# Kernel optimization log

Measured on AMD Instinct MI355X. Metric: run time of the kernel, lower is better.

## Reference

```python
import jax, jax.numpy as jnp
import numpy as np

BATCH, SEQ, D_IN, D_OUT, PALETTE = 4, 2048, 4096, 4096, 256


def setup_inputs() -> dict:
    key = jax.random.key(0)
    k_in, k_w, k_lut, k_b = jax.random.split(key, 4)
    inp = jax.random.normal(k_in, (BATCH, SEQ, D_IN), dtype=jnp.float32)
    # palette indices playing the role of the stored uint8 weight tensor
    weight = jax.random.randint(k_w, (D_OUT, D_IN), 0, PALETTE, dtype=jnp.int32)
    # fp8-derived palette values (simulated as small fp32 centroids)
    lookup_table = jax.random.normal(k_lut, (PALETTE,), dtype=jnp.float32) * 0.02
    bias = jax.random.normal(k_b, (D_OUT,), dtype=jnp.float32) * 0.01
    return {"input": inp, "lookup_table": lookup_table, "weight": weight, "bias": bias}


def reference(input, lookup_table, weight, bias):
    # Dequantize palette indices -> full weight matrix [D_OUT, D_IN]
    full_weights = lookup_table[weight]
    # F.linear: input @ W^T + bias
    out = jnp.einsum("bsd,od->bso", input, full_weights)
    return out + bias
```

## Files before the change

kernel.cpp:

```cpp
#include <hip/hip_runtime.h>
#include <cstdint>


static constexpr int Md = 8192;
static constexpr int Nd = 4096;
static constexpr int Kd = 4096;

typedef _Float16 half8 __attribute__((ext_vector_type(8)));
typedef float f32x4 __attribute__((ext_vector_type(4)));

__device__ __forceinline__ void async_copy16(const _Float16* g, _Float16* l) {
  __builtin_amdgcn_global_load_lds((const __attribute__((address_space(1))) void*)g,
                                   (__attribute__((address_space(3))) void*)l, 16, 0, 0);
}

__global__ __launch_bounds__(256) void cvt_a(const float* __restrict__ in,
                                             _Float16* __restrict__ out) {
  const size_t i = (size_t)blockIdx.x * 256 + threadIdx.x;
  const float4 x = ((const float4*)in)[2 * i];
  const float4 y = ((const float4*)in)[2 * i + 1];
  half8 h;
  h[0] = (_Float16)x.x; h[1] = (_Float16)x.y; h[2] = (_Float16)x.z; h[3] = (_Float16)x.w;
  h[4] = (_Float16)y.x; h[5] = (_Float16)y.y; h[6] = (_Float16)y.z; h[7] = (_Float16)y.w;
  *(half8*)(out + 8 * i) = h;
}

__global__ __launch_bounds__(256) void dequant_b(const int* __restrict__ w,
                                                 const float* __restrict__ lut,
                                                 _Float16* __restrict__ out) {
  __shared__ float slut[256];
  slut[threadIdx.x] = lut[threadIdx.x];
  __syncthreads();
  const size_t i = (size_t)blockIdx.x * 256 + threadIdx.x;
  const int4 a = ((const int4*)w)[2 * i];
  const int4 b = ((const int4*)w)[2 * i + 1];
  half8 h;
  h[0] = (_Float16)slut[a.x]; h[1] = (_Float16)slut[a.y];
  h[2] = (_Float16)slut[a.z]; h[3] = (_Float16)slut[a.w];
  h[4] = (_Float16)slut[b.x]; h[5] = (_Float16)slut[b.y];
  h[6] = (_Float16)slut[b.z]; h[7] = (_Float16)slut[b.w];
  *(half8*)(out + 8 * i) = h;
}

__global__ __launch_bounds__(256) void gemm_f16(const _Float16* __restrict__ A,
                                                const _Float16* __restrict__ Bt,
                                                const float* __restrict__ bias,
                                                float* __restrict__ C) {
  __shared__ __align__(16) _Float16 As[128 * 64];
  __shared__ __align__(16) _Float16 Bs[128 * 64];

  const int tid = threadIdx.x;
  const int lane = tid & 63;
  const int wave = tid >> 6;
  const int wm = wave >> 1;
  const int wn = wave & 1;
  const int bm = blockIdx.x, bn = blockIdx.y;

  const int sr = wave * 8 + (lane >> 3);
  const int gc = ((lane & 7) ^ (sr & 7)) * 8;
  const _Float16* ag = A  + (size_t)(bm * 128 + sr) * Kd + gc;
  const _Float16* bg = Bt + (size_t)(bn * 128 + sr) * Kd + gc;
  _Float16* al = As + sr * 64 + (lane & 7) * 8;
  _Float16* bl = Bs + sr * 64 + (lane & 7) * 8;

  const int fr = lane & 15;
  const int fq = lane >> 4;
  const int e = fr & 7;
  const int slot0 = (fq ^ e) * 8;
  const int slot1 = ((4 | fq) ^ e) * 8;
  const _Float16* afp = As + (wm * 64 + fr) * 64;
  const _Float16* bfp = Bs + (wn * 64 + fr) * 64;

  f32x4 acc[4][4] = {};

  for (int kt = 0; kt < Kd / 64; ++kt) {
#pragma unroll
    for (int r = 0; r < 4; ++r) {
      async_copy16(ag + (size_t)r * 32 * Kd, al + r * 2048);
      async_copy16(bg + (size_t)r * 32 * Kd, bl + r * 2048);
    }
    ag += 64;
    bg += 64;
    __syncthreads();
#pragma unroll
    for (int ks = 0; ks < 2; ++ks) {
      const int slot = ks ? slot1 : slot0;
      half8 a[4], b[4];
#pragma unroll
      for (int i = 0; i < 4; ++i) a[i] = *(const half8*)(afp + i * 16 * 64 + slot);
#pragma unroll
      for (int j = 0; j < 4; ++j) b[j] = *(const half8*)(bfp + j * 16 * 64 + slot);
#pragma unroll
      for (int i = 0; i < 4; ++i)
#pragma unroll
        for (int j = 0; j < 4; ++j)
          acc[i][j] = __builtin_amdgcn_mfma_f32_16x16x32_f16(a[i], b[j], acc[i][j], 0, 0, 0);
    }
    __syncthreads();
  }

  const int ccol0 = bn * 128 + wn * 64 + fr;
  const int crow0 = bm * 128 + wm * 64 + fq * 4;
  float bv[4];
#pragma unroll
  for (int j = 0; j < 4; ++j) bv[j] = bias[ccol0 + j * 16];
#pragma unroll
  for (int i = 0; i < 4; ++i) {
#pragma unroll
    for (int r = 0; r < 4; ++r) {
      float* cp = C + (size_t)(crow0 + i * 16 + r) * Nd + ccol0;
#pragma unroll
      for (int j = 0; j < 4; ++j) cp[j * 16] = acc[i][j][r] + bv[j];
    }
  }
}

extern "C" void kernel_launch(void* const* d_in, const int* in_sizes, int n_in,
                              void* d_out, int out_size, void* d_ws, size_t ws_size,
                              hipStream_t stream) {
  const float* inp  = (const float*)d_in[0];
  const float* lut  = (const float*)d_in[1];
  const int*   wgt  = (const int*)d_in[2];
  const float* bias = (const float*)d_in[3];
  float* out = (float*)d_out;

  _Float16* Ah = (_Float16*)d_ws;
  _Float16* Bh = (_Float16*)d_ws + (size_t)Md * Kd;

  cvt_a<<<(Md * (size_t)Kd) / (8 * 256), 256, 0, stream>>>(inp, Ah);
  dequant_b<<<((size_t)Nd * Kd) / (8 * 256), 256, 0, stream>>>(wgt, lut, Bh);

  dim3 grid(Md / 128, Nd / 128);
  gemm_f16<<<grid, 256, 0, stream>>>(Ah, Bh, bias, out);
}
```

Before: 547.5 us.

## Use 256x256 tiles with double-buffered LDS and ping-pong MFMA scheduling

Replaces the 128x128 single-buffered GEMM with a 256x256 block tile of 512 threads. The LDS is double-buffered, so the next K-tile's async global-to-LDS copy is issued before the current tile is computed, with explicit waitcnt and barriers. The MFMA work is split into four quadrant phases with setprio so loads and matrix ops from the two resident blocks interleave, and a block-index remap groups blocks for L2 locality. The larger tile increases data reuse per loaded byte, at the cost of 128 KB of LDS per block, more accumulator registers, and many extra barriers.

```diff
diff --git a/kernel.cpp b/kernel.cpp
--- a/kernel.cpp
+++ b/kernel.cpp
@@ -5,6 +5,7 @@
 static constexpr int Md = 8192;
 static constexpr int Nd = 4096;
 static constexpr int Kd = 4096;
+static constexpr int NKT = Kd / 64;
 
 typedef _Float16 half8 __attribute__((ext_vector_type(8)));
 typedef float f32x4 __attribute__((ext_vector_type(4)));
@@ -42,70 +43,147 @@
   *(half8*)(out + 8 * i) = h;
 }
 
-__global__ __launch_bounds__(256) void gemm_f16(const _Float16* __restrict__ A,
-                                                const _Float16* __restrict__ Bt,
-                                                const float* __restrict__ bias,
-                                                float* __restrict__ C) {
-  __shared__ __align__(16) _Float16 As[128 * 64];
-  __shared__ __align__(16) _Float16 Bs[128 * 64];
+__global__ __launch_bounds__(512, 2) void gemm_f16(const _Float16* __restrict__ A,
+                                                   const _Float16* __restrict__ Bt,
+                                                   const float* __restrict__ bias,
+                                                   float* __restrict__ C) {
+  __shared__ __align__(16) _Float16 As[2][256 * 64];
+  __shared__ __align__(16) _Float16 Bs[2][256 * 64];
 
   const int tid = threadIdx.x;
   const int lane = tid & 63;
   const int wave = tid >> 6;
-  const int wm = wave >> 1;
-  const int wn = wave & 1;
-  const int bm = blockIdx.x, bn = blockIdx.y;
-
-  const int sr = wave * 8 + (lane >> 3);
-  const int gc = ((lane & 7) ^ (sr & 7)) * 8;
-  const _Float16* ag = A  + (size_t)(bm * 128 + sr) * Kd + gc;
-  const _Float16* bg = Bt + (size_t)(bn * 128 + sr) * Kd + gc;
-  _Float16* al = As + sr * 64 + (lane & 7) * 8;
-  _Float16* bl = Bs + sr * 64 + (lane & 7) * 8;
+  const int wm = wave >> 2;
+  const int wn = wave & 3;
+
+  const int bid0 = blockIdx.x + blockIdx.y * gridDim.x;
+  const int bid = (bid0 & 7) * 64 + (bid0 >> 3);
+  const int bm = bid & 31;
+  const int bn = bid >> 5;
+
+  const int trow = tid >> 3;
+  const int tcol = tid & 7;
+  const int gch = tcol ^ (trow & 7);
+  const _Float16* ag = A + (size_t)(bm * 256 + trow) * Kd + gch * 8;
+  const _Float16* bg = Bt + (size_t)(bn * 256 + trow) * Kd + gch * 8;
+  const int lds_off = trow * 64 + tcol * 8;
+
+  auto stage = [&](int buf, int kt) {
+#pragma unroll
+    for (int ht = 0; ht < 4; ++ht) {
+      async_copy16(ag + (size_t)kt * 64 + (size_t)ht * (64 * Kd),
+                   &As[buf][lds_off + ht * 4096]);
+      async_copy16(bg + (size_t)kt * 64 + (size_t)ht * (64 * Kd),
+                   &Bs[buf][lds_off + ht * 4096]);
+    }
+  };
 
   const int fr = lane & 15;
   const int fq = lane >> 4;
   const int e = fr & 7;
-  const int slot0 = (fq ^ e) * 8;
-  const int slot1 = ((4 | fq) ^ e) * 8;
-  const _Float16* afp = As + (wm * 64 + fr) * 64;
-  const _Float16* bfp = Bs + (wn * 64 + fr) * 64;
-
-  f32x4 acc[4][4] = {};
-
-  for (int kt = 0; kt < Kd / 64; ++kt) {
-#pragma unroll
-    for (int r = 0; r < 4; ++r) {
-      async_copy16(ag + (size_t)r * 32 * Kd, al + r * 2048);
-      async_copy16(bg + (size_t)r * 32 * Kd, bl + r * 2048);
-    }
-    ag += 64;
-    bg += 64;
-    __syncthreads();
-#pragma unroll
-    for (int ks = 0; ks < 2; ++ks) {
-      const int slot = ks ? slot1 : slot0;
-      half8 a[4], b[4];
-#pragma unroll
-      for (int i = 0; i < 4; ++i) a[i] = *(const half8*)(afp + i * 16 * 64 + slot);
-#pragma unroll
-      for (int j = 0; j < 4; ++j) b[j] = *(const half8*)(bfp + j * 16 * 64 + slot);
-#pragma unroll
-      for (int i = 0; i < 4; ++i)
-#pragma unroll
-        for (int j = 0; j < 4; ++j)
-          acc[i][j] = __builtin_amdgcn_mfma_f32_16x16x32_f16(a[i], b[j], acc[i][j], 0, 0, 0);
-    }
-    __syncthreads();
+  const int s0 = (fq ^ e) * 8;
+  const int s1 = ((4 | fq) ^ e) * 8;
+
+  f32x4 acc[8][4] = {};
+
+  stage(0, 0);
+
+  for (int kt = 0; kt < NKT; ++kt) {
+    const int cur = kt & 1;
+    if (kt + 1 < NKT) {
+      stage(cur ^ 1, kt + 1);
+      asm volatile("s_waitcnt vmcnt(8)" ::: "memory");
+    } else {
+      asm volatile("s_waitcnt vmcnt(0)" ::: "memory");
+    }
+    __builtin_amdgcn_s_barrier();
+
+    const _Float16* as = &As[cur][(wm * 128 + fr) * 64];
+    const _Float16* bs = &Bs[cur][(wn * 64 + fr) * 64];
+
+    half8 a[4][2], b0[2][2], b1[2][2];
+
+#pragma unroll
+    for (int i = 0; i < 4; ++i) {
+      a[i][0] = *(const half8*)(as + i * 16 * 64 + s0);
+      a[i][1] = *(const half8*)(as + i * 16 * 64 + s1);
+    }
+#pragma unroll
+    for (int j = 0; j < 2; ++j) {
+      b0[j][0] = *(const half8*)(bs + j * 16 * 64 + s0);
+      b0[j][1] = *(const half8*)(bs + j * 16 * 64 + s1);
+    }
+    __builtin_amdgcn_s_barrier();
+    asm volatile("s_waitcnt lgkmcnt(0)" ::: "memory");
+    __builtin_amdgcn_sched_barrier(0);
+    __builtin_amdgcn_s_setprio(1);
+#pragma unroll
+    for (int i = 0; i < 4; ++i)
+#pragma unroll
+      for (int j = 0; j < 2; ++j) {
+        acc[i][j] = __builtin_amdgcn_mfma_f32_16x16x32_f16(a[i][0], b0[j][0], acc[i][j], 0, 0, 0);
+        acc[i][j] = __builtin_amdgcn_mfma_f32_16x16x32_f16(a[i][1], b0[j][1], acc[i][j], 0, 0, 0);
+      }
+    __builtin_amdgcn_s_setprio(0);
+    __builtin_amdgcn_s_barrier();
+
+#pragma unroll
+    for (int j = 0; j < 2; ++j) {
+      b1[j][0] = *(const half8*)(bs + (32 + j * 16) * 64 + s0);
+      b1[j][1] = *(const half8*)(bs + (32 + j * 16) * 64 + s1);
+    }
+    __builtin_amdgcn_s_barrier();
+    asm volatile("s_waitcnt lgkmcnt(0)" ::: "memory");
+    __builtin_amdgcn_sched_barrier(0);
+    __builtin_amdgcn_s_setprio(1);
+#pragma unroll
+    for (int i = 0; i < 4; ++i)
+#pragma unroll
+      for (int j = 0; j < 2; ++j) {
+        acc[i][2 + j] = __builtin_amdgcn_mfma_f32_16x16x32_f16(a[i][0], b1[j][0], acc[i][2 + j], 0, 0, 0);
+        acc[i][2 + j] = __builtin_amdgcn_mfma_f32_16x16x32_f16(a[i][1], b1[j][1], acc[i][2 + j], 0, 0, 0);
+      }
+    __builtin_amdgcn_s_setprio(0);
+    __builtin_amdgcn_s_barrier();
+
+#pragma unroll
+    for (int i = 0; i < 4; ++i) {
+      a[i][0] = *(const half8*)(as + (64 + i * 16) * 64 + s0);
+      a[i][1] = *(const half8*)(as + (64 + i * 16) * 64 + s1);
+    }
+    __builtin_amdgcn_s_barrier();
+    asm volatile("s_waitcnt lgkmcnt(0)" ::: "memory");
+    __builtin_amdgcn_sched_barrier(0);
+    __builtin_amdgcn_s_setprio(1);
+#pragma unroll
+    for (int i = 0; i < 4; ++i)
+#pragma unroll
+      for (int j = 0; j < 2; ++j) {
+        acc[4 + i][2 + j] = __builtin_amdgcn_mfma_f32_16x16x32_f16(a[i][0], b1[j][0], acc[4 + i][2 + j], 0, 0, 0);
+        acc[4 + i][2 + j] = __builtin_amdgcn_mfma_f32_16x16x32_f16(a[i][1], b1[j][1], acc[4 + i][2 + j], 0, 0, 0);
+      }
+    __builtin_amdgcn_s_setprio(0);
+    __builtin_amdgcn_s_barrier();
+
+    __builtin_amdgcn_s_setprio(1);
+#pragma unroll
+    for (int i = 0; i < 4; ++i)
+#pragma unroll
+      for (int j = 0; j < 2; ++j) {
+        acc[4 + i][j] = __builtin_amdgcn_mfma_f32_16x16x32_f16(a[i][0], b0[j][0], acc[4 + i][j], 0, 0, 0);
+        acc[4 + i][j] = __builtin_amdgcn_mfma_f32_16x16x32_f16(a[i][1], b0[j][1], acc[4 + i][j], 0, 0, 0);
+      }
+    __builtin_amdgcn_s_setprio(0);
+    __builtin_amdgcn_s_barrier();
   }
 
-  const int ccol0 = bn * 128 + wn * 64 + fr;
-  const int crow0 = bm * 128 + wm * 64 + fq * 4;
+  const int ccol0 = bn * 256 + wn * 64 + fr;
+  const int crow0 = bm * 256 + wm * 128 + fq * 4;
   float bv[4];
 #pragma unroll
   for (int j = 0; j < 4; ++j) bv[j] = bias[ccol0 + j * 16];
 #pragma unroll
-  for (int i = 0; i < 4; ++i) {
+  for (int i = 0; i < 8; ++i) {
 #pragma unroll
     for (int r = 0; r < 4; ++r) {
       float* cp = C + (size_t)(crow0 + i * 16 + r) * Nd + ccol0;
@@ -118,9 +196,9 @@
 extern "C" void kernel_launch(void* const* d_in, const int* in_sizes, int n_in,
                               void* d_out, int out_size, void* d_ws, size_t ws_size,
                               hipStream_t stream) {
-  const float* inp  = (const float*)d_in[0];
-  const float* lut  = (const float*)d_in[1];
-  const int*   wgt  = (const int*)d_in[2];
+  const float* inp = (const float*)d_in[0];
+  const float* lut = (const float*)d_in[1];
+  const int* wgt = (const int*)d_in[2];
   const float* bias = (const float*)d_in[3];
   float* out = (float*)d_out;
 
@@ -130,6 +208,6 @@
   cvt_a<<<(Md * (size_t)Kd) / (8 * 256), 256, 0, stream>>>(inp, Ah);
   dequant_b<<<((size_t)Nd * Kd) / (8 * 256), 256, 0, stream>>>(wgt, lut, Bh);
 
-  dim3 grid(Md / 128, Nd / 128);
-  gemm_f16<<<grid, 256, 0, stream>>>(Ah, Bh, bias, out);
-}
+  dim3 grid(Md / 256, Nd / 256);
+  gemm_f16<<<grid, 512, 0, stream>>>(Ah, Bh, bias, out);
+}
```

Result: slower. 583.5 us (+6.6%).
